# Kernel tuning notes

Hardware: AMD Instinct MI355X
Metric: run time of the kernel (lower is better)

The kernel has to match this reference:

```python
import jax, jax.numpy as jnp
import numpy as np

B, S, D_IN, D_OUT = 4, 2048, 1024, 1024


def setup_inputs() -> dict:
    key = jax.random.key(0)
    k1, k2, k3, k4 = jax.random.split(key, 4)
    x = jax.random.normal(k1, (B, S, D_IN), dtype=jnp.float32)
    # torch nn.Linear weight layout: [d_out, d_in]
    wq = jax.random.normal(k2, (D_OUT, D_IN), dtype=jnp.float32) * (1.0 / np.sqrt(D_IN))
    wk = jax.random.normal(k3, (D_OUT, D_IN), dtype=jnp.float32) * (1.0 / np.sqrt(D_IN))
    wv = jax.random.normal(k4, (D_OUT, D_IN), dtype=jnp.float32) * (1.0 / np.sqrt(D_IN))
    return {"x": x, "wq": wq, "wk": wk, "wv": wv}


def reference(x, wq, wk, wv):
    # q,k,v: [b, s, d_out]
    q = jnp.einsum('bsd,od->bso', x, wq)
    k = jnp.einsum('bsd,od->bso', x, wk)
    v = jnp.einsum('bsd,od->bso', x, wv)
    scale = 1.0 / jnp.sqrt(jnp.asarray(k.shape[-1], dtype=q.dtype))
    scores = jnp.einsum('bqd,bkd->bqk', q, k)  # [b, s, s]
    s = scores.shape[-1]
    causal = jnp.tril(jnp.ones((s, s), dtype=bool))
    scores = jnp.where(causal, scores, -jnp.inf)
    attn = jax.nn.softmax(scores * scale, axis=-1)
    # dropout p=0.0 -> identity
    return jnp.einsum('bqk,bkd->bqd', attn, v)
```

## Files before the change

### kernel.cpp

```cpp
#include <hip/hip_runtime.h>
#include <hip/hip_bf16.h>
#include <cstdint>

#define BATCH 4
#define SEQ   2048
#define DIN   1024
#define DOUT  1024
#define SCALE 0.03125f

typedef unsigned short u16;
typedef float  f32x4  __attribute__((ext_vector_type(4)));
typedef __bf16 bf16x8 __attribute__((ext_vector_type(8)));

__device__ __forceinline__ u16 f2bf(float f) {
    unsigned u = __float_as_uint(f);
    unsigned r = 0x7fffu + ((u >> 16) & 1u);
    return (u16)((u + r) >> 16);
}

__device__ __forceinline__ f32x4 mfma16(bf16x8 a, bf16x8 b, f32x4 c) {
    return __builtin_amdgcn_mfma_f32_16x16x32_bf16(a, b, c, 0, 0, 0);
}

__device__ __forceinline__ void gl_lds16(const u16* g, u16* l) {
    __builtin_amdgcn_global_load_lds(
        (const __attribute__((address_space(1))) unsigned int*)g,
        (__attribute__((address_space(3))) unsigned int*)l, 16, 0, 0);
}

#define BAR    asm volatile("s_barrier" ::: "memory")
#define VMCNT4 asm volatile("s_waitcnt vmcnt(4)" ::: "memory")
#define VMCNT0 asm volatile("s_waitcnt vmcnt(0)" ::: "memory")
#define LGKM0  asm volatile("s_waitcnt lgkmcnt(0)" ::: "memory")

__global__ __launch_bounds__(256) void cvt_all(const float* __restrict__ x,
                                               const float* __restrict__ wq,
                                               const float* __restrict__ wk,
                                               const float* __restrict__ wv,
                                               u16* __restrict__ dst) {
    const size_t NX = (size_t)BATCH * SEQ * DIN;
    size_t e = ((size_t)blockIdx.x * 256 + threadIdx.x) * 8;
    const float* src;
    size_t off;
    if (e < NX) { src = x; off = e; }
    else {
        size_t r = e - NX;
        int w = (int)(r >> 20);
        src = (w == 0) ? wq : (w == 1) ? wk : wv;
        off = r & ((1u << 20) - 1);
    }
    f32x4 a = *(const f32x4*)(src + off);
    f32x4 b = *(const f32x4*)(src + off + 4);
    uint4 o;
    o.x = (unsigned)f2bf(a[0]) | ((unsigned)f2bf(a[1]) << 16);
    o.y = (unsigned)f2bf(a[2]) | ((unsigned)f2bf(a[3]) << 16);
    o.z = (unsigned)f2bf(b[0]) | ((unsigned)f2bf(b[1]) << 16);
    o.w = (unsigned)f2bf(b[2]) | ((unsigned)f2bf(b[3]) << 16);
    *(uint4*)(dst + e) = o;
}

__device__ __forceinline__ void stg128(const u16* __restrict__ g, int ld,
                                       u16* unit, int tid) {
#pragma unroll
    for (int i = 0; i < 2; i++) {
        int D = (i * 512 + tid) * 16;
        int r = D >> 7, w = D & 127;
        int gcol = (w ^ ((r & 7) << 4)) >> 1;
        gl_lds16(g + (size_t)r * ld + gcol, unit + (i * 512 + (tid >> 6) * 64) * 8);
    }
}

__device__ __forceinline__ void rd4(const u16* unit, int rowbase, int l15, int l4,
                                    bf16x8 f[4][2]) {
    const char* u = (const char*)unit;
#pragma unroll
    for (int i = 0; i < 4; i++) {
        int row = rowbase + i * 16 + l15;
#pragma unroll
        for (int kk = 0; kk < 2; kk++)
            f[i][kk] = *(const bf16x8*)(u + row * 128 +
                                        ((kk * 64 + l4 * 16) ^ ((row & 7) << 4)));
    }
}

__device__ __forceinline__ void rd2k(const u16* unit, int row0, int l15, int l4,
                                     bf16x8 f[2]) {
    const char* u = (const char*)unit;
    int row = row0 + l15;
#pragma unroll
    for (int kk = 0; kk < 2; kk++)
        f[kk] = *(const bf16x8*)(u + row * 128 +
                                 ((kk * 64 + l4 * 16) ^ ((row & 7) << 4)));
}

__device__ __forceinline__ void g64_body(u16* lds, const u16* __restrict__ Ag,
                                         int lda, const u16* __restrict__ Bg,
                                         int ldb, int nkt, int wm, int wn,
                                         int l15, int l4, int tid,
                                         f32x4 acc[4][2]) {
    bf16x8 a[4][2], b0[2], b1[2];
    u16* A0 = lds;          u16* B0 = lds + 8192;
    u16* A1 = lds + 16384;  u16* B1 = lds + 24576;
    stg128(Ag, lda, A0, tid);      stg128(Bg, ldb, B0, tid);
    stg128(Ag + 64, lda, A1, tid); stg128(Bg + 64, ldb, B1, tid);
    VMCNT4; BAR;
    for (int t = 0; t < nkt; t += 2) {
        {
            const int k2 = ((t + 2 < nkt) ? t + 2 : nkt - 1) * 64;
            rd4(A0, wm * 64, l15, l4, a);
            rd2k(B0, wn * 32, l15, l4, b0);
            rd2k(B0, wn * 32 + 16, l15, l4, b1);
            BAR;
            __builtin_amdgcn_s_setprio(1);
#pragma unroll
            for (int kk = 0; kk < 2; kk++)
#pragma unroll
                for (int mi = 0; mi < 4; mi++)
                    acc[mi][0] = mfma16(a[mi][kk], b0[kk], acc[mi][0]);
            __builtin_amdgcn_s_setprio(0);
            LGKM0; BAR;
            stg128(Ag + k2, lda, A0, tid);
            stg128(Bg + k2, ldb, B0, tid);
            VMCNT4; BAR;
            __builtin_amdgcn_s_setprio(1);
#pragma unroll
            for (int kk = 0; kk < 2; kk++)
#pragma unroll
                for (int mi = 0; mi < 4; mi++)
                    acc[mi][1] = mfma16(a[mi][kk], b1[kk], acc[mi][1]);
            __builtin_amdgcn_s_setprio(0);
            BAR;
        }
        {
            const int k3 = ((t + 3 < nkt) ? t + 3 : nkt - 1) * 64;
            rd4(A1, wm * 64, l15, l4, a);
            rd2k(B1, wn * 32, l15, l4, b0);
            rd2k(B1, wn * 32 + 16, l15, l4, b1);
            BAR;
            __builtin_amdgcn_s_setprio(1);
#pragma unroll
            for (int kk = 0; kk < 2; kk++)
#pragma unroll
                for (int mi = 0; mi < 4; mi++)
                    acc[mi][0] = mfma16(a[mi][kk], b0[kk], acc[mi][0]);
            __builtin_amdgcn_s_setprio(0);
            LGKM0; BAR;
            stg128(Ag + k3, lda, A1, tid);
            stg128(Bg + k3, ldb, B1, tid);
            VMCNT4; BAR;
            __builtin_amdgcn_s_setprio(1);
#pragma unroll
            for (int kk = 0; kk < 2; kk++)
#pragma unroll
                for (int mi = 0; mi < 4; mi++)
                    acc[mi][1] = mfma16(a[mi][kk], b1[kk], acc[mi][1]);
            __builtin_amdgcn_s_setprio(0);
            BAR;
        }
    }
    VMCNT0;
}

__device__ __forceinline__ void stg_half(const u16* __restrict__ gbase,
                                         u16* unit, int tid) {
#pragma unroll
    for (int i = 0; i < 2; i++) {
        int D = (i * 512 + tid) * 16;
        int r = D >> 7, w = D & 127;
        int gcol = (w ^ ((r & 7) << 4)) >> 1;
        gl_lds16(gbase + (size_t)r * DIN + gcol,
                 unit + (i * 512 + (tid >> 6) * 64) * 8);
    }
}

__device__ __forceinline__ void rdA8(const u16* unit, int mh, int l15, int l4,
                                     int sw, bf16x8 a[4][2]) {
    const char* u = (const char*)unit;
#pragma unroll
    for (int mi = 0; mi < 4; mi++)
#pragma unroll
        for (int kk = 0; kk < 2; kk++)
            a[mi][kk] = *(const bf16x8*)(u + (mh * 64 + mi * 16 + l15) * 128 +
                                         ((kk * 64 + l4 * 16) ^ sw));
}

__device__ __forceinline__ void rdB8(const u16* unit, int wn1, int nh, int l15,
                                     int l4, int sw, bf16x8 b[2][2]) {
    const char* u = (const char*)unit;
#pragma unroll
    for (int ni = 0; ni < 2; ni++)
#pragma unroll
        for (int kk = 0; kk < 2; kk++)
            b[ni][kk] = *(const bf16x8*)(u + (wn1 * 64 + nh * 32 + ni * 16 + l15) * 128 +
                                         ((kk * 64 + l4 * 16) ^ sw));
}

#define QUAD(MH, NH)                                                         \
    __builtin_amdgcn_s_setprio(1);                                           \
    _Pragma("unroll") for (int kk = 0; kk < 2; kk++)                         \
    _Pragma("unroll") for (int mi = 0; mi < 4; mi++)                         \
    _Pragma("unroll") for (int ni = 0; ni < 2; ni++)                         \
        acc[(MH)*4 + mi][(NH)*2 + ni] =                                      \
            mfma16(a[mi][kk], bb[NH][ni][kk], acc[(MH)*4 + mi][(NH)*2 + ni]);\
    __builtin_amdgcn_s_setprio(0);

__global__ __launch_bounds__(512) void qkv_gemm256(const u16* __restrict__ xb,
                                                   const u16* __restrict__ wb,
                                                   u16* __restrict__ qkv) {
    extern __shared__ __align__(16) u16 lds[];
    const int tid = threadIdx.x, lane = tid & 63, wid = tid >> 6;
    const int wm = wid >> 2, wn = wid & 3, bh = wn >> 1, wn1 = wn & 1;
    const int l15 = lane & 15, l4 = lane >> 4;
    const int sw = (l15 & 7) << 4;

    u16* A00 = lds;              u16* A01 = lds + 8192;
    u16* A10 = lds + 16384;      u16* A11 = lds + 24576;
    u16* B00 = lds + 32768;      u16* B01 = lds + 40960;
    u16* B10 = lds + 49152;      u16* B11 = lds + 57344;
    u16* Ar0 = lds + wm * 8192;
    u16* Ar1 = lds + 16384 + wm * 8192;
    u16* Br0 = lds + 32768 + bh * 8192;
    u16* Br1 = lds + 49152 + bh * 8192;

    for (int tile = blockIdx.x; tile < 384; tile += 256) {
        const int wg = (tile & 7) * 48 + (tile >> 3);
        const int mt = wg & 31, nt = wg >> 5;
        const int m0 = mt * 256, n0 = nt * 256;
        const u16* Ag = xb + (size_t)m0 * DIN;
        const u16* Bg = wb + (size_t)n0 * DIN;
        f32x4 acc[8][4] = {};
        bf16x8 a[4][2], bb[2][2][2];

        stg_half(Bg,                          B00, tid);
        stg_half(Bg + (size_t)128 * DIN,      B01, tid);
        stg_half(Ag,                          A00, tid);
        stg_half(Ag + (size_t)128 * DIN,      A01, tid);
        stg_half(Bg + 64,                     B10, tid);
        stg_half(Bg + (size_t)128 * DIN + 64, B11, tid);
        VMCNT4; BAR;

        for (int i = 0; i < 8; i++) {
            const int t1k = (2 * i + 1) * 64;
            const int k2 = ((2 * i + 2 < 16) ? 2 * i + 2 : 15) * 64;
            const int k3 = ((2 * i + 3 < 16) ? 2 * i + 3 : 15) * 64;
            rdA8(Ar0, 0, l15, l4, sw, a);
            rdB8(Br0, wn1, 0, l15, l4, sw, bb[0]);
            stg_half(Ag + t1k, A10, tid);
            BAR; QUAD(0, 0); BAR;
            rdB8(Br0, wn1, 1, l15, l4, sw, bb[1]);
            stg_half(Ag + (size_t)128 * DIN + t1k, A11, tid);
            BAR; QUAD(0, 1); BAR;
            rdA8(Ar0, 1, l15, l4, sw, a);
            stg_half(Bg + k2, B00, tid);
            BAR; QUAD(1, 0); BAR;
            stg_half(Bg + (size_t)128 * DIN + k2, B01, tid);
            VMCNT4; BAR; QUAD(1, 1); BAR;
            rdA8(Ar1, 0, l15, l4, sw, a);
            rdB8(Br1, wn1, 0, l15, l4, sw, bb[0]);
            stg_half(Ag + k2, A00, tid);
            BAR; QUAD(0, 0); BAR;
            rdB8(Br1, wn1, 1, l15, l4, sw, bb[1]);
            stg_half(Ag + (size_t)128 * DIN + k2, A01, tid);
            BAR; QUAD(0, 1); BAR;
            rdA8(Ar1, 1, l15, l4, sw, a);
            stg_half(Bg + k3, B10, tid);
            BAR; QUAD(1, 0); BAR;
            stg_half(Bg + (size_t)128 * DIN + k3, B11, tid);
            VMCNT4; BAR; QUAD(1, 1); BAR;
        }
        VMCNT0;

        const int wsel = n0 >> 10, c0 = n0 & 1023;
        u16* Op = qkv + (size_t)wsel * ((size_t)BATCH * SEQ * DOUT);
#pragma unroll
        for (int ai = 0; ai < 8; ai++)
#pragma unroll
            for (int bj = 0; bj < 4; bj++)
#pragma unroll
                for (int rr = 0; rr < 4; rr++) {
                    int row = m0 + wm * 128 + ai * 16 + l4 * 4 + rr;
                    int col = c0 + wn * 64 + bj * 16 + l15;
                    Op[(size_t)row * DOUT + col] = f2bf(acc[ai][bj][rr]);
                }
    }
}

__global__ __launch_bounds__(256) void vtrans(const u16* __restrict__ v,
                                              u16* __restrict__ vt) {
    __shared__ __align__(16) u16 t[64][80];
    const int s0 = blockIdx.x * 64, d0 = blockIdx.y * 64;
    const size_t bo = (size_t)blockIdx.z * SEQ * DOUT;
    const int tid = threadIdx.x;
#pragma unroll
    for (int i = 0; i < 2; i++) {
        int e = (tid + i * 256) * 8;
        int r = e >> 6, c = e & 63;
        *(uint4*)&t[r][c] = *(const uint4*)&v[bo + (size_t)(s0 + r) * DOUT + d0 + c];
    }
    __syncthreads();
#pragma unroll
    for (int i = 0; i < 2; i++) {
        int e = (tid + i * 256) * 8;
        int rd = e >> 6, cs = e & 63;
        u16 tmp[8];
#pragma unroll
        for (int j = 0; j < 8; j++) tmp[j] = t[cs + j][rd];
        uint4 o;
        o.x = (unsigned)tmp[0] | ((unsigned)tmp[1] << 16);
        o.y = (unsigned)tmp[2] | ((unsigned)tmp[3] << 16);
        o.z = (unsigned)tmp[4] | ((unsigned)tmp[5] << 16);
        o.w = (unsigned)tmp[6] | ((unsigned)tmp[7] << 16);
        *(uint4*)&vt[(size_t)blockIdx.z * DOUT * SEQ + (size_t)(d0 + rd) * SEQ + s0 + cs] = o;
    }
}

__global__ __launch_bounds__(512) void qk_g64(const u16* __restrict__ qg,
                                              const u16* __restrict__ kg,
                                              u16* __restrict__ sg,
                                              float* __restrict__ rowsum) {
    extern __shared__ __align__(16) u16 lds[];
    const int bxx = blockIdx.x, batch = blockIdx.y;
    int mt = 0, base = 0;
#pragma unroll 16
    for (int m = 0; m < 16; m++) {
        int c = m + 1;
        if (bxx < base + c) { mt = m; break; }
        base += c;
    }
    const int nt = bxx - base;
    const int m0 = mt * 128, n0 = nt * 128;
    const int tid = threadIdx.x, lane = tid & 63;
    const int wm = (tid >> 6) >> 2, wn = (tid >> 6) & 3;
    const int l15 = lane & 15, l4 = lane >> 4;
    const size_t bo = (size_t)batch * SEQ * DOUT;

    f32x4 acc[4][2] = {};
    g64_body(lds, qg + bo + (size_t)m0 * DOUT, DOUT,
             kg + bo + (size_t)n0 * DOUT, DOUT, 16,
             wm, wn, l15, l4, tid, acc);

    u16* Sp = sg + (size_t)batch * SEQ * SEQ;
    float* Rs = rowsum + (size_t)batch * SEQ;
#pragma unroll
    for (int ai = 0; ai < 4; ai++)
#pragma unroll
        for (int rr = 0; rr < 4; rr++) {
            int q = m0 + wm * 64 + ai * 16 + l4 * 4 + rr;
            float rp = 0.f;
#pragma unroll
            for (int bj = 0; bj < 2; bj++) {
                int kc = n0 + wn * 32 + bj * 16 + l15;
                float p = (kc <= q) ? __expf(acc[ai][bj][rr] * SCALE) : 0.f;
                rp += p;
                Sp[(size_t)q * SEQ + kc] = f2bf(p);
            }
#pragma unroll
            for (int off = 8; off >= 1; off >>= 1) rp += __shfl_xor(rp, off, 16);
            if (l15 == 0) atomicAdd(&Rs[q], rp);
        }
}

__global__ __launch_bounds__(512) void pv_g64(const u16* __restrict__ pg,
                                              const u16* __restrict__ vtg,
                                              const float* __restrict__ rowsum,
                                              float* __restrict__ og) {
    extern __shared__ __align__(16) u16 lds[];
    const int pr = blockIdx.x;
    const int n0 = blockIdx.y * 128, batch = blockIdx.z;
    const int tid = threadIdx.x, lane = tid & 63;
    const int wm = (tid >> 6) >> 2, wn = (tid >> 6) & 3;
    const int l15 = lane & 15, l4 = lane >> 4;
    const u16* Pb = pg + (size_t)batch * SEQ * SEQ;
    const u16* Vb = vtg + (size_t)batch * DOUT * SEQ + (size_t)n0 * SEQ;
    const float* Rs = rowsum + (size_t)batch * SEQ;
    float* Ob = og + (size_t)batch * SEQ * DOUT;

#pragma unroll
    for (int half = 0; half < 2; half++) {
        const int mt = half ? (15 - pr) : pr;
        const int m0 = mt * 128;
        f32x4 acc[4][2] = {};
        g64_body(lds, Pb + (size_t)m0 * SEQ, SEQ, Vb, SEQ, (mt + 1) * 2,
                 wm, wn, l15, l4, tid, acc);
#pragma unroll
        for (int ai = 0; ai < 4; ai++)
#pragma unroll
            for (int rr = 0; rr < 4; rr++) {
                int q = m0 + wm * 64 + ai * 16 + l4 * 4 + rr;
                float inv = 1.0f / Rs[q];
#pragma unroll
                for (int bj = 0; bj < 2; bj++) {
                    int d = n0 + wn * 32 + bj * 16 + l15;
                    Ob[(size_t)q * DOUT + d] = acc[ai][bj][rr] * inv;
                }
            }
    }
}

extern "C" void kernel_launch(void* const* d_in, const int* in_sizes, int n_in,
                              void* d_out, int out_size, void* d_ws, size_t ws_size,
                              hipStream_t stream) {
    const float* x  = (const float*)d_in[0];
    const float* wq = (const float*)d_in[1];
    const float* wk = (const float*)d_in[2];
    const float* wv = (const float*)d_in[3];
    float* out = (float*)d_out;

    const size_t NX  = (size_t)BATCH * SEQ * DIN;
    const size_t NWT = (size_t)DOUT * DIN;
    u16* xb  = (u16*)d_ws;
    u16* wb  = xb + NX;
    u16* qkv = wb + 3 * NWT;
    u16* vt  = qkv + 3 * NX;
    u16* sb  = vt + NX;
    float* rowsum = (float*)(sb + (size_t)BATCH * SEQ * SEQ);

    cvt_all<<<(NX + 3 * NWT) / 8 / 256, 256, 0, stream>>>(x, wq, wk, wv, xb);

    (void)hipMemsetAsync(rowsum, 0, (size_t)BATCH * SEQ * sizeof(float), stream);

    (void)hipFuncSetAttribute((const void*)qkv_gemm256,
                              hipFuncAttributeMaxDynamicSharedMemorySize, 131072);
    (void)hipFuncSetAttribute((const void*)qk_g64,
                              hipFuncAttributeMaxDynamicSharedMemorySize, 65536);
    (void)hipFuncSetAttribute((const void*)pv_g64,
                              hipFuncAttributeMaxDynamicSharedMemorySize, 65536);

    qkv_gemm256<<<dim3(256), dim3(512), 131072, stream>>>(xb, wb, qkv);

    vtrans<<<dim3(SEQ / 64, DOUT / 64, BATCH), 256, 0, stream>>>(qkv + 2 * NX, vt);

    qk_g64<<<dim3(136, BATCH), dim3(512), 65536, stream>>>(qkv, qkv + NX, sb, rowsum);

    pv_g64<<<dim3(8, 8, 4), dim3(512), 65536, stream>>>(sb, vt, rowsum, out);
}
```

Baseline: 168.4 us.

## Retile QKV GEMM to 256x192 tiles for balanced two-wave scheduling

Changes the fused QKV projection GEMM from 256x256 to 256x192 output tiles, so the 3072-wide output splits into 512 tiles that fill exactly two waves of 256 workgroups instead of leaving the second wave half empty. The LDS staging is reorganised to a 192-row B buffer per k-step, with a new two-phase pipeline and adjusted wait counts. Output columns may now straddle the Q/K/V boundary, so the destination is chosen per column. Each tile reuses the A operand less, which adds some extra global traffic.

```diff
diff --git a/kernel.cpp b/kernel.cpp
--- a/kernel.cpp
+++ b/kernel.cpp
@@ -29,6 +29,7 @@
 }
 
 #define BAR    asm volatile("s_barrier" ::: "memory")
+#define VMCNT3 asm volatile("s_waitcnt vmcnt(3)" ::: "memory")
 #define VMCNT4 asm volatile("s_waitcnt vmcnt(4)" ::: "memory")
 #define VMCNT0 asm volatile("s_waitcnt vmcnt(0)" ::: "memory")
 #define LGKM0  asm volatile("s_waitcnt lgkmcnt(0)" ::: "memory")
@@ -70,11 +71,35 @@
     }
 }
 
+__device__ __forceinline__ void stg192(const u16* __restrict__ g, int ld,
+                                       u16* unit, int tid) {
+#pragma unroll
+    for (int i = 0; i < 3; i++) {
+        int D = (i * 512 + tid) * 16;
+        int r = D >> 7, w = D & 127;
+        int gcol = (w ^ ((r & 7) << 4)) >> 1;
+        gl_lds16(g + (size_t)r * ld + gcol, unit + (i * 512 + (tid >> 6) * 64) * 8);
+    }
+}
+
 __device__ __forceinline__ void rd4(const u16* unit, int rowbase, int l15, int l4,
                                     bf16x8 f[4][2]) {
     const char* u = (const char*)unit;
 #pragma unroll
     for (int i = 0; i < 4; i++) {
+        int row = rowbase + i * 16 + l15;
+#pragma unroll
+        for (int kk = 0; kk < 2; kk++)
+            f[i][kk] = *(const bf16x8*)(u + row * 128 +
+                                        ((kk * 64 + l4 * 16) ^ ((row & 7) << 4)));
+    }
+}
+
+__device__ __forceinline__ void rd3(const u16* unit, int rowbase, int l15, int l4,
+                                    bf16x8 f[3][2]) {
+    const char* u = (const char*)unit;
+#pragma unroll
+    for (int i = 0; i < 3; i++) {
         int row = rowbase + i * 16 + l15;
 #pragma unroll
         for (int kk = 0; kk < 2; kk++)
@@ -161,126 +186,89 @@
     VMCNT0;
 }
 
-__device__ __forceinline__ void stg_half(const u16* __restrict__ gbase,
-                                         u16* unit, int tid) {
-#pragma unroll
-    for (int i = 0; i < 2; i++) {
-        int D = (i * 512 + tid) * 16;
-        int r = D >> 7, w = D & 127;
-        int gcol = (w ^ ((r & 7) << 4)) >> 1;
-        gl_lds16(gbase + (size_t)r * DIN + gcol,
-                 unit + (i * 512 + (tid >> 6) * 64) * 8);
-    }
-}
-
 __device__ __forceinline__ void rdA8(const u16* unit, int mh, int l15, int l4,
-                                     int sw, bf16x8 a[4][2]) {
-    const char* u = (const char*)unit;
-#pragma unroll
-    for (int mi = 0; mi < 4; mi++)
-#pragma unroll
-        for (int kk = 0; kk < 2; kk++)
-            a[mi][kk] = *(const bf16x8*)(u + (mh * 64 + mi * 16 + l15) * 128 +
-                                         ((kk * 64 + l4 * 16) ^ sw));
-}
-
-__device__ __forceinline__ void rdB8(const u16* unit, int wn1, int nh, int l15,
-                                     int l4, int sw, bf16x8 b[2][2]) {
-    const char* u = (const char*)unit;
-#pragma unroll
-    for (int ni = 0; ni < 2; ni++)
-#pragma unroll
-        for (int kk = 0; kk < 2; kk++)
-            b[ni][kk] = *(const bf16x8*)(u + (wn1 * 64 + nh * 32 + ni * 16 + l15) * 128 +
-                                         ((kk * 64 + l4 * 16) ^ sw));
-}
-
-#define QUAD(MH, NH)                                                         \
+                                     bf16x8 a[4][2]) {
+    rd4(unit, mh * 64, l15, l4, a);
+}
+
+#define QKV_PH0(AU, BU, ANX0, ANX1, K1)                                      \
+    rdA8((AU), 0, l15, l4, a);                                               \
+    rd3((BU), wn * 48, l15, l4, b);                                          \
+    stg128(Ag + (K1), DIN, (ANX0), tid);                                     \
+    stg128(Ag + (size_t)128 * DIN + (K1), DIN, (ANX1), tid);                 \
+    BAR;                                                                     \
     __builtin_amdgcn_s_setprio(1);                                           \
     _Pragma("unroll") for (int kk = 0; kk < 2; kk++)                         \
     _Pragma("unroll") for (int mi = 0; mi < 4; mi++)                         \
-    _Pragma("unroll") for (int ni = 0; ni < 2; ni++)                         \
-        acc[(MH)*4 + mi][(NH)*2 + ni] =                                      \
-            mfma16(a[mi][kk], bb[NH][ni][kk], acc[(MH)*4 + mi][(NH)*2 + ni]);\
-    __builtin_amdgcn_s_setprio(0);
-
-__global__ __launch_bounds__(512) void qkv_gemm256(const u16* __restrict__ xb,
+    _Pragma("unroll") for (int ni = 0; ni < 3; ni++)                         \
+        acc[mi][ni] = mfma16(a[mi][kk], b[ni][kk], acc[mi][ni]);             \
+    __builtin_amdgcn_s_setprio(0);                                           \
+    BAR;
+
+#define QKV_PH1(AU, BCUR, K2)                                                \
+    rdA8((AU), 1, l15, l4, a);                                               \
+    stg192(Bg + (K2), DIN, (BCUR), tid);                                     \
+    VMCNT3; BAR;                                                             \
+    __builtin_amdgcn_s_setprio(1);                                           \
+    _Pragma("unroll") for (int kk = 0; kk < 2; kk++)                         \
+    _Pragma("unroll") for (int mi = 0; mi < 4; mi++)                         \
+    _Pragma("unroll") for (int ni = 0; ni < 3; ni++)                         \
+        acc[4 + mi][ni] = mfma16(a[mi][kk], b[ni][kk], acc[4 + mi][ni]);     \
+    __builtin_amdgcn_s_setprio(0);                                           \
+    BAR;
+
+__global__ __launch_bounds__(512) void qkv_gemm192(const u16* __restrict__ xb,
                                                    const u16* __restrict__ wb,
                                                    u16* __restrict__ qkv) {
     extern __shared__ __align__(16) u16 lds[];
     const int tid = threadIdx.x, lane = tid & 63, wid = tid >> 6;
-    const int wm = wid >> 2, wn = wid & 3, bh = wn >> 1, wn1 = wn & 1;
+    const int wm = wid >> 2, wn = wid & 3;
     const int l15 = lane & 15, l4 = lane >> 4;
-    const int sw = (l15 & 7) << 4;
-
-    u16* A00 = lds;              u16* A01 = lds + 8192;
-    u16* A10 = lds + 16384;      u16* A11 = lds + 24576;
-    u16* B00 = lds + 32768;      u16* B01 = lds + 40960;
-    u16* B10 = lds + 49152;      u16* B11 = lds + 57344;
+
+    u16* A00 = lds;          u16* A01 = lds + 8192;
+    u16* A10 = lds + 16384;  u16* A11 = lds + 24576;
+    u16* B0  = lds + 32768;  u16* B1  = lds + 45056;
     u16* Ar0 = lds + wm * 8192;
     u16* Ar1 = lds + 16384 + wm * 8192;
-    u16* Br0 = lds + 32768 + bh * 8192;
-    u16* Br1 = lds + 49152 + bh * 8192;
-
-    for (int tile = blockIdx.x; tile < 384; tile += 256) {
-        const int wg = (tile & 7) * 48 + (tile >> 3);
+
+    for (int tile = blockIdx.x; tile < 512; tile += 256) {
+        const int wg = (tile & 7) * 64 + (tile >> 3);
         const int mt = wg & 31, nt = wg >> 5;
-        const int m0 = mt * 256, n0 = nt * 256;
+        const int m0 = mt * 256, n0 = nt * 192;
         const u16* Ag = xb + (size_t)m0 * DIN;
         const u16* Bg = wb + (size_t)n0 * DIN;
-        f32x4 acc[8][4] = {};
-        bf16x8 a[4][2], bb[2][2][2];
-
-        stg_half(Bg,                          B00, tid);
-        stg_half(Bg + (size_t)128 * DIN,      B01, tid);
-        stg_half(Ag,                          A00, tid);
-        stg_half(Ag + (size_t)128 * DIN,      A01, tid);
-        stg_half(Bg + 64,                     B10, tid);
-        stg_half(Bg + (size_t)128 * DIN + 64, B11, tid);
-        VMCNT4; BAR;
+        f32x4 acc[8][3] = {};
+        bf16x8 a[4][2], b[3][2];
+
+        stg128(Ag, DIN, A00, tid);
+        stg128(Ag + (size_t)128 * DIN, DIN, A01, tid);
+        stg192(Bg, DIN, B0, tid);
+        stg192(Bg + 64, DIN, B1, tid);
+        VMCNT3;
+        BAR;
 
         for (int i = 0; i < 8; i++) {
-            const int t1k = (2 * i + 1) * 64;
+            const int k1 = (2 * i + 1) * 64;
             const int k2 = ((2 * i + 2 < 16) ? 2 * i + 2 : 15) * 64;
             const int k3 = ((2 * i + 3 < 16) ? 2 * i + 3 : 15) * 64;
-            rdA8(Ar0, 0, l15, l4, sw, a);
-            rdB8(Br0, wn1, 0, l15, l4, sw, bb[0]);
-            stg_half(Ag + t1k, A10, tid);
-            BAR; QUAD(0, 0); BAR;
-            rdB8(Br0, wn1, 1, l15, l4, sw, bb[1]);
-            stg_half(Ag + (size_t)128 * DIN + t1k, A11, tid);
-            BAR; QUAD(0, 1); BAR;
-            rdA8(Ar0, 1, l15, l4, sw, a);
-            stg_half(Bg + k2, B00, tid);
-            BAR; QUAD(1, 0); BAR;
-            stg_half(Bg + (size_t)128 * DIN + k2, B01, tid);
-            VMCNT4; BAR; QUAD(1, 1); BAR;
-            rdA8(Ar1, 0, l15, l4, sw, a);
-            rdB8(Br1, wn1, 0, l15, l4, sw, bb[0]);
-            stg_half(Ag + k2, A00, tid);
-            BAR; QUAD(0, 0); BAR;
-            rdB8(Br1, wn1, 1, l15, l4, sw, bb[1]);
-            stg_half(Ag + (size_t)128 * DIN + k2, A01, tid);
-            BAR; QUAD(0, 1); BAR;
-            rdA8(Ar1, 1, l15, l4, sw, a);
-            stg_half(Bg + k3, B10, tid);
-            BAR; QUAD(1, 0); BAR;
-            stg_half(Bg + (size_t)128 * DIN + k3, B11, tid);
-            VMCNT4; BAR; QUAD(1, 1); BAR;
+            QKV_PH0(Ar0, B0, A10, A11, k1)
+            QKV_PH1(Ar0, B0, k2)
+            QKV_PH0(Ar1, B1, A00, A01, k2)
+            QKV_PH1(Ar1, B1, k3)
         }
         VMCNT0;
 
-        const int wsel = n0 >> 10, c0 = n0 & 1023;
-        u16* Op = qkv + (size_t)wsel * ((size_t)BATCH * SEQ * DOUT);
 #pragma unroll
         for (int ai = 0; ai < 8; ai++)
 #pragma unroll
-            for (int bj = 0; bj < 4; bj++)
+            for (int bj = 0; bj < 3; bj++)
 #pragma unroll
                 for (int rr = 0; rr < 4; rr++) {
                     int row = m0 + wm * 128 + ai * 16 + l4 * 4 + rr;
-                    int col = c0 + wn * 64 + bj * 16 + l15;
-                    Op[(size_t)row * DOUT + col] = f2bf(acc[ai][bj][rr]);
+                    int col = n0 + wn * 48 + bj * 16 + l15;
+                    int wsel = col >> 10;
+                    u16* Op = qkv + (size_t)wsel * ((size_t)BATCH * SEQ * DOUT);
+                    Op[(size_t)row * DOUT + (col & 1023)] = f2bf(acc[ai][bj][rr]);
                 }
     }
 }
@@ -419,14 +407,14 @@
 
     (void)hipMemsetAsync(rowsum, 0, (size_t)BATCH * SEQ * sizeof(float), stream);
 
-    (void)hipFuncSetAttribute((const void*)qkv_gemm256,
-                              hipFuncAttributeMaxDynamicSharedMemorySize, 131072);
+    (void)hipFuncSetAttribute((const void*)qkv_gemm192,
+                              hipFuncAttributeMaxDynamicSharedMemorySize, 114688);
     (void)hipFuncSetAttribute((const void*)qk_g64,
                               hipFuncAttributeMaxDynamicSharedMemorySize, 65536);
     (void)hipFuncSetAttribute((const void*)pv_g64,
                               hipFuncAttributeMaxDynamicSharedMemorySize, 65536);
 
-    qkv_gemm256<<<dim3(256), dim3(512), 131072, stream>>>(xb, wb, qkv);
+    qkv_gemm192<<<dim3(256), dim3(512), 114688, stream>>>(xb, wb, qkv);
 
     vtrans<<<dim3(SEQ / 64, DOUT / 64, BATCH), 256, 0, stream>>>(qkv + 2 * NX, vt);
 
```

After: 160.7 us. 4.6% less time.
